# Kernel optimization log

Hardware: AMD Instinct MI355X
Metric: run time of the kernel (lower is better)

## Reference

```python
import jax, jax.numpy as jnp
import numpy as np

N = 8192
IN_DIM = 256
OUT_DIM = 256


def setup_inputs() -> dict:
    key = jax.random.key(0)
    k1, k2, k3, k4 = jax.random.split(key, 4)
    x = jax.random.normal(k1, (N, IN_DIM), dtype=jnp.float32)
    adj = jax.random.uniform(k2, (N, N), dtype=jnp.float32)
    # nn.Linear(in_dim, out_dim): weight [out,in], bias [out]. Store W as [in,out].
    bound = 1.0 / np.sqrt(IN_DIM)
    W = jax.random.uniform(k3, (IN_DIM, OUT_DIM), dtype=jnp.float32, minval=-bound, maxval=bound)
    b = jax.random.uniform(k4, (OUT_DIM,), dtype=jnp.float32, minval=-bound, maxval=bound)
    return {"x": x, "adj": adj, "W": W, "b": b}


def reference(x, adj, W, b):
    # ReLU( D^{-1/2} (A + I) D^{-1/2} X W + b )
    # A_hat = adj + I; degree = A_hat.sum(axis=1)
    n = adj.shape[0]
    A_hat = adj + jnp.eye(n, dtype=adj.dtype)
    degree = A_hat.sum(axis=1)
    d_inv_sqrt = degree ** -0.5  # [N]
    # D^{-1/2} @ A_hat @ D^{-1/2} == row-scale then col-scale (no NxN diag matmuls)
    A_norm = A_hat * d_inv_sqrt[:, None] * d_inv_sqrt[None, :]
    out = A_norm @ x          # [N, in_dim]
    out = out @ W + b         # [N, out_dim]
    return jax.nn.relu(out)
```

## Files before the change

### kernel.cpp

```cpp
#include <hip/hip_runtime.h>
#include <hip/hip_bf16.h>


typedef __attribute__((ext_vector_type(8))) short short8;
typedef __attribute__((ext_vector_type(4))) float floatx4;

#define GLDS16(g, l) __builtin_amdgcn_global_load_lds(\
    (const __attribute__((address_space(1))) void*)(g), \
    (__attribute__((address_space(3))) void*)(l), 16, 0, 0)

__device__ __forceinline__ unsigned short f2b(float f) {
  unsigned int x = __builtin_bit_cast(unsigned int, f);
  unsigned int r = (x + 0x7fffu + ((x >> 16) & 1u)) >> 16;
  return (unsigned short)r;
}

__global__ __launch_bounds__(256) void k_prep(
    const float* __restrict__ adj, float* __restrict__ degree,
    unsigned short* __restrict__ adjb) {
  __shared__ float red[256];
  const int t = threadIdx.x;
  const int bg = blockIdx.x >> 2, kq = blockIdx.x & 3;
  const int m0 = bg * 32;
  const int row = m0 + (t & 31);
  const int kc = t >> 5;
  const float* src = adj + (size_t)row * 8192 + kq * 2048 + kc * 8;
  unsigned short* dst = adjb +
      ((((size_t)(row >> 6)) * 128 + kq * 32) * 512 + kc * 64 + (row & 63)) * 8;
  float rs = 0.f;
#pragma unroll 4
  for (int kt = 0; kt < 32; ++kt) {
    float4 a = *(const float4*)(src + kt * 64);
    float4 b = *(const float4*)(src + kt * 64 + 4);
    rs += a.x + a.y + a.z + a.w + b.x + b.y + b.z + b.w;
    short8 u;
    u[0] = (short)f2b(a.x); u[1] = (short)f2b(a.y);
    u[2] = (short)f2b(a.z); u[3] = (short)f2b(a.w);
    u[4] = (short)f2b(b.x); u[5] = (short)f2b(b.y);
    u[6] = (short)f2b(b.z); u[7] = (short)f2b(b.w);
    *(short8*)(dst + (size_t)kt * 512 * 8) = u;
  }
  red[t] = rs;
  __syncthreads();
  if (t < 32) {
    float sum = red[t] + red[t + 32] + red[t + 64] + red[t + 96] +
                red[t + 128] + red[t + 160] + red[t + 192] + red[t + 224];
    atomicAdd(degree + m0 + t, sum);
  }
}

__global__ __launch_bounds__(256) void k_xw(
    const float* __restrict__ X, const float* __restrict__ W,
    const float* __restrict__ bias, const float* __restrict__ degree,
    float* __restrict__ Zd, unsigned short* __restrict__ Zsb) {
  __shared__ unsigned short ldsT[256 * 36];
  const int t = threadIdx.x, l = t & 63, w = t >> 6;
  const int m0 = blockIdx.x * 32;
  const int r0 = w * 8;
  const int n0 = l * 4;
  const float* Xp = X + (size_t)(m0 + r0) * 256;
  float acc[8][4] = {};
#pragma unroll 2
  for (int k = 0; k < 256; k += 4) {
    float4 wv[4];
#pragma unroll
    for (int j = 0; j < 4; ++j) wv[j] = *(const float4*)(W + (size_t)(k + j) * 256 + n0);
#pragma unroll
    for (int r = 0; r < 8; ++r) {
      float4 xv = *(const float4*)(Xp + r * 256 + k);
      const float xs[4] = {xv.x, xv.y, xv.z, xv.w};
#pragma unroll
      for (int j = 0; j < 4; ++j) {
        acc[r][0] += xs[j] * wv[j].x;
        acc[r][1] += xs[j] * wv[j].y;
        acc[r][2] += xs[j] * wv[j].z;
        acc[r][3] += xs[j] * wv[j].w;
      }
    }
  }
  const float4 bv = *(const float4*)(bias + n0);
  const int kt = m0 >> 6, hh = (m0 >> 5) & 1;
#pragma unroll
  for (int r = 0; r < 8; ++r) {
    const int row = m0 + r0 + r;
    const float sr = rsqrtf(degree[row] + 1.0f);
    float4 zd;
    zd.x = sr * sr * acc[r][0] + bv.x;
    zd.y = sr * sr * acc[r][1] + bv.y;
    zd.z = sr * sr * acc[r][2] + bv.z;
    zd.w = sr * sr * acc[r][3] + bv.w;
    *(float4*)(Zd + (size_t)row * 256 + n0) = zd;
#pragma unroll
    for (int n = 0; n < 4; ++n)
      ldsT[(size_t)(n0 + n) * 36 + (r0 + r)] = f2b(sr * acc[r][n]);
  }
  __syncthreads();
#pragma unroll
  for (int c = 0; c < 4; ++c) {
    const unsigned short* p = ldsT + (size_t)t * 36 + c * 8;
    short8 vv;
#pragma unroll
    for (int j = 0; j < 8; ++j) vv[j] = p[j];
    *(short8*)(Zsb + ((size_t)kt * 2048 + (hh * 4 + c) * 256 + t) * 8) = vv;
  }
}

__global__ __launch_bounds__(512) void k_main(
    const unsigned short* __restrict__ adjb, const unsigned short* __restrict__ Zsb,
    float* __restrict__ P0, float* __restrict__ P1) {
  __shared__ __align__(16) char lds[2][24576];
  const int t = threadIdx.x, l = t & 63, w = t >> 6;
  const int quad = l >> 4, nl = l & 15;
  const int bm = blockIdx.x >> 2, sk = (blockIdx.x >> 1) & 1, nh = blockIdx.x & 1;
  const int wm = w & 1, wn = w >> 1;
  const unsigned short* aBase = adjb + ((size_t)bm * 128 + sk * 64) * 512 * 8;
  const int sl0 = t, sl1 = 512 + t;
  const size_t bU0 = (size_t)(sl0 >> 7) * 256 + nh * 128 + (sl0 & 127);
  const size_t bU1 = (size_t)(sl1 >> 7) * 256 + nh * 128 + (sl1 & 127);
  floatx4 acc[2][2] = {};

  GLDS16(aBase + (size_t)t * 8, lds[0] + t * 16);
  GLDS16(Zsb + ((size_t)(sk * 64) * 2048 + bU0) * 8, lds[0] + 8192 + sl0 * 16);
  GLDS16(Zsb + ((size_t)(sk * 64) * 2048 + bU1) * 8, lds[0] + 8192 + sl1 * 16);
  __syncthreads();

  for (int kt = 0; kt < 64; ++kt) {
    const int cur = kt & 1, nxt = cur ^ 1;
    const int ktn = kt < 63 ? kt + 1 : 63;
    GLDS16(aBase + ((size_t)ktn * 512 + t) * 8, lds[nxt] + t * 16);
    GLDS16(Zsb + ((size_t)(sk * 64 + ktn) * 2048 + bU0) * 8, lds[nxt] + 8192 + sl0 * 16);
    GLDS16(Zsb + ((size_t)(sk * 64 + ktn) * 2048 + bU1) * 8, lds[nxt] + 8192 + sl1 * 16);
    const char* rA = lds[cur];
    const char* rB = lds[cur] + 8192;
#pragma unroll
    for (int kk = 0; kk < 2; ++kk) {
      const int kc = kk * 4 + quad;
      short8 af[2], bf[2];
      af[0] = *(const short8*)(rA + (kc * 64 + wm * 32 + nl) * 16);
      af[1] = *(const short8*)(rA + (kc * 64 + wm * 32 + 16 + nl) * 16);
      bf[0] = *(const short8*)(rB + (kc * 128 + wn * 32 + nl) * 16);
      bf[1] = *(const short8*)(rB + (kc * 128 + wn * 32 + 16 + nl) * 16);
      acc[0][0] = __builtin_amdgcn_mfma_f32_16x16x32_bf16(af[0], bf[0], acc[0][0], 0, 0, 0);
      acc[0][1] = __builtin_amdgcn_mfma_f32_16x16x32_bf16(af[0], bf[1], acc[0][1], 0, 0, 0);
      acc[1][0] = __builtin_amdgcn_mfma_f32_16x16x32_bf16(af[1], bf[0], acc[1][0], 0, 0, 0);
      acc[1][1] = __builtin_amdgcn_mfma_f32_16x16x32_bf16(af[1], bf[1], acc[1][1], 0, 0, 0);
    }
    __syncthreads();
  }

  float* P = sk ? P1 : P0;
#pragma unroll
  for (int mi = 0; mi < 2; ++mi)
#pragma unroll
    for (int ni = 0; ni < 2; ++ni)
#pragma unroll
      for (int r = 0; r < 4; ++r) {
        const int row = bm * 64 + wm * 32 + mi * 16 + quad * 4 + r;
        const int col = nh * 128 + wn * 32 + ni * 16 + nl;
        P[(size_t)row * 256 + col] = acc[mi][ni][r];
      }
}

__global__ __launch_bounds__(256) void k_fin(
    const float* __restrict__ P0, const float* __restrict__ P1,
    const float* __restrict__ Zd, const float* __restrict__ degree,
    float* __restrict__ out) {
  const int i = blockIdx.x * 256 + threadIdx.x;
  const int row = i >> 6;
  const float sr = rsqrtf(degree[row] + 1.0f);
  const float4 p0 = *(const float4*)(P0 + (size_t)i * 4);
  const float4 p1 = *(const float4*)(P1 + (size_t)i * 4);
  const float4 zd = *(const float4*)(Zd + (size_t)i * 4);
  float4 v;
  v.x = sr * (p0.x + p1.x) + zd.x;
  v.y = sr * (p0.y + p1.y) + zd.y;
  v.z = sr * (p0.z + p1.z) + zd.z;
  v.w = sr * (p0.w + p1.w) + zd.w;
  v.x = v.x > 0.f ? v.x : 0.f;
  v.y = v.y > 0.f ? v.y : 0.f;
  v.z = v.z > 0.f ? v.z : 0.f;
  v.w = v.w > 0.f ? v.w : 0.f;
  *(float4*)(out + (size_t)i * 4) = v;
}

extern "C" void kernel_launch(void* const* d_in, const int* in_sizes, int n_in,
                              void* d_out, int out_size, void* d_ws, size_t ws_size,
                              hipStream_t stream) {
  const float* X    = (const float*)d_in[0];
  const float* adj  = (const float*)d_in[1];
  const float* W    = (const float*)d_in[2];
  const float* bias = (const float*)d_in[3];
  float* out = (float*)d_out;
  char* ws = (char*)d_ws;

  float* degree        = (float*)(ws);
  float* Zd            = (float*)(ws + (1 << 20));
  unsigned short* Zsb  = (unsigned short*)(ws + (9 << 20));
  float* P0            = (float*)(ws + (13 << 20));
  float* P1            = (float*)(ws + (21 << 20));
  unsigned short* adjb = (unsigned short*)(ws + ((size_t)29 << 20));

  hipMemsetAsync(degree, 0, 8192 * sizeof(float), stream);
  hipLaunchKernelGGL(k_prep, dim3(1024), dim3(256), 0, stream, adj, degree, adjb);
  hipLaunchKernelGGL(k_xw, dim3(256), dim3(256), 0, stream, X, W, bias, degree, Zd, Zsb);
  hipLaunchKernelGGL(k_main, dim3(512), dim3(512), 0, stream, adjb, Zsb, P0, P1);
  hipLaunchKernelGGL(k_fin, dim3(2048), dim3(256), 0, stream, P0, P1, Zd, degree, out);
}
```

Baseline: 526.5 us.

## Fuse fp32-to-bf16 adjacency conversion into GEMM loads, drop bf16 adj copy

The prep kernel that converted the 256MB fp32 adjacency into a tiled bf16 copy is replaced by a degree-only row-sum kernel using warp shuffles, with no atomics or memset. The main GEMM now reads fp32 adj directly, converts it to bf16 in registers and writes it to a padded LDS layout, with a register prefetch two steps ahead. The work split changes from 2 K-splits by 2 N-halves to 4 K-splits covering all 256 columns, so each adj tile is read once. The aim is to remove the extra write and read of the bf16 adj copy. The cost is that adj is now read twice (degree pass and GEMM), and there are four partial buffers to reduce in the final kernel.

Measured after the change: 509.1 us. -3.3%, faster.

```diff
diff --git a/kernel.cpp b/kernel.cpp
--- a/kernel.cpp
+++ b/kernel.cpp
@@ -15,38 +15,21 @@
   return (unsigned short)r;
 }
 
-__global__ __launch_bounds__(256) void k_prep(
-    const float* __restrict__ adj, float* __restrict__ degree,
-    unsigned short* __restrict__ adjb) {
-  __shared__ float red[256];
+__global__ __launch_bounds__(256) void k_deg(
+    const float* __restrict__ adj, float* __restrict__ degree) {
   const int t = threadIdx.x;
-  const int bg = blockIdx.x >> 2, kq = blockIdx.x & 3;
-  const int m0 = bg * 32;
-  const int row = m0 + (t & 31);
-  const int kc = t >> 5;
-  const float* src = adj + (size_t)row * 8192 + kq * 2048 + kc * 8;
-  unsigned short* dst = adjb +
-      ((((size_t)(row >> 6)) * 128 + kq * 32) * 512 + kc * 64 + (row & 63)) * 8;
+  const int row = blockIdx.x * 8 + (t >> 5);
+  const int c = t & 31;
+  const float* src = adj + (size_t)row * 8192 + c * 4;
   float rs = 0.f;
-#pragma unroll 4
-  for (int kt = 0; kt < 32; ++kt) {
-    float4 a = *(const float4*)(src + kt * 64);
-    float4 b = *(const float4*)(src + kt * 64 + 4);
-    rs += a.x + a.y + a.z + a.w + b.x + b.y + b.z + b.w;
-    short8 u;
-    u[0] = (short)f2b(a.x); u[1] = (short)f2b(a.y);
-    u[2] = (short)f2b(a.z); u[3] = (short)f2b(a.w);
-    u[4] = (short)f2b(b.x); u[5] = (short)f2b(b.y);
-    u[6] = (short)f2b(b.z); u[7] = (short)f2b(b.w);
-    *(short8*)(dst + (size_t)kt * 512 * 8) = u;
-  }
-  red[t] = rs;
-  __syncthreads();
-  if (t < 32) {
-    float sum = red[t] + red[t + 32] + red[t + 64] + red[t + 96] +
-                red[t + 128] + red[t + 160] + red[t + 192] + red[t + 224];
-    atomicAdd(degree + m0 + t, sum);
-  }
+#pragma unroll 8
+  for (int it = 0; it < 64; ++it) {
+    float4 v = *(const float4*)(src + it * 128);
+    rs += v.x + v.y + v.z + v.w;
+  }
+#pragma unroll
+  for (int o = 16; o > 0; o >>= 1) rs += __shfl_down(rs, o, 32);
+  if (c == 0) degree[row] = rs;
 }
 
 __global__ __launch_bounds__(256) void k_xw(
@@ -97,85 +80,110 @@
   __syncthreads();
 #pragma unroll
   for (int c = 0; c < 4; ++c) {
+    const int kcv = hh * 4 + c;
     const unsigned short* p = ldsT + (size_t)t * 36 + c * 8;
     short8 vv;
 #pragma unroll
     for (int j = 0; j < 8; ++j) vv[j] = p[j];
-    *(short8*)(Zsb + ((size_t)kt * 2048 + (hh * 4 + c) * 256 + t) * 8) = vv;
+    *(short8*)(Zsb + ((size_t)kt * 2048 + kcv * 256 + t) * 8) = vv;
   }
 }
 
 __global__ __launch_bounds__(512) void k_main(
-    const unsigned short* __restrict__ adjb, const unsigned short* __restrict__ Zsb,
-    float* __restrict__ P0, float* __restrict__ P1) {
-  __shared__ __align__(16) char lds[2][24576];
+    const float* __restrict__ adj, const unsigned short* __restrict__ Zsb,
+    float* __restrict__ P) {
+  __shared__ __align__(16) char lds[2][20608];
   const int t = threadIdx.x, l = t & 63, w = t >> 6;
   const int quad = l >> 4, nl = l & 15;
-  const int bm = blockIdx.x >> 2, sk = (blockIdx.x >> 1) & 1, nh = blockIdx.x & 1;
+  const int bm = blockIdx.x >> 2, sk = blockIdx.x & 3;
+  const int m0 = bm * 64;
   const int wm = w & 1, wn = w >> 1;
-  const unsigned short* aBase = adjb + ((size_t)bm * 128 + sk * 64) * 512 * 8;
-  const int sl0 = t, sl1 = 512 + t;
-  const size_t bU0 = (size_t)(sl0 >> 7) * 256 + nh * 128 + (sl0 & 127);
-  const size_t bU1 = (size_t)(sl1 >> 7) * 256 + nh * 128 + (sl1 & 127);
-  floatx4 acc[2][2] = {};
-
-  GLDS16(aBase + (size_t)t * 8, lds[0] + t * 16);
-  GLDS16(Zsb + ((size_t)(sk * 64) * 2048 + bU0) * 8, lds[0] + 8192 + sl0 * 16);
-  GLDS16(Zsb + ((size_t)(sk * 64) * 2048 + bU1) * 8, lds[0] + 8192 + sl1 * 16);
+  const int aRow = t >> 3, aCol = t & 7;
+  const float* aSrc = adj + (size_t)(m0 + aRow) * 8192 + sk * 2048 + aCol * 4;
+  const int aOff = (aCol >> 1) * 1040 + aRow * 16 + (aCol & 1) * 8;
+  const unsigned short* bBase = Zsb + (size_t)sk * 65536 * 8;
+  floatx4 acc[2][4] = {};
+
+  float4 avP = *(const float4*)(aSrc);
+#pragma unroll
+  for (int q = 0; q < 2; ++q) {
+    const int sl = q * 512 + t;
+    GLDS16(bBase + (size_t)sl * 8, lds[0] + 4224 + sl * 16);
+  }
+  {
+    unsigned short u0 = f2b(avP.x), u1 = f2b(avP.y), u2 = f2b(avP.z), u3 = f2b(avP.w);
+    unsigned long long pk = (unsigned long long)u0 | ((unsigned long long)u1 << 16)
+                          | ((unsigned long long)u2 << 32) | ((unsigned long long)u3 << 48);
+    *(unsigned long long*)(lds[0] + aOff) = pk;
+  }
+  avP = *(const float4*)(aSrc + 32);
   __syncthreads();
 
-  for (int kt = 0; kt < 64; ++kt) {
-    const int cur = kt & 1, nxt = cur ^ 1;
-    const int ktn = kt < 63 ? kt + 1 : 63;
-    GLDS16(aBase + ((size_t)ktn * 512 + t) * 8, lds[nxt] + t * 16);
-    GLDS16(Zsb + ((size_t)(sk * 64 + ktn) * 2048 + bU0) * 8, lds[nxt] + 8192 + sl0 * 16);
-    GLDS16(Zsb + ((size_t)(sk * 64 + ktn) * 2048 + bU1) * 8, lds[nxt] + 8192 + sl1 * 16);
+  for (int i = 0; i < 64; ++i) {
+    const int cur = i & 1, nxt = cur ^ 1;
+    const int ib = i < 63 ? i + 1 : 63;
+    const int ia = i < 62 ? i + 2 : 63;
+#pragma unroll
+    for (int q = 0; q < 2; ++q) {
+      const int sl = q * 512 + t;
+      GLDS16(bBase + (size_t)(ib * 1024 + sl) * 8, lds[nxt] + 4224 + sl * 16);
+    }
+    float4 avN = *(const float4*)(aSrc + ia * 32);
     const char* rA = lds[cur];
-    const char* rB = lds[cur] + 8192;
-#pragma unroll
-    for (int kk = 0; kk < 2; ++kk) {
-      const int kc = kk * 4 + quad;
-      short8 af[2], bf[2];
-      af[0] = *(const short8*)(rA + (kc * 64 + wm * 32 + nl) * 16);
-      af[1] = *(const short8*)(rA + (kc * 64 + wm * 32 + 16 + nl) * 16);
-      bf[0] = *(const short8*)(rB + (kc * 128 + wn * 32 + nl) * 16);
-      bf[1] = *(const short8*)(rB + (kc * 128 + wn * 32 + 16 + nl) * 16);
-      acc[0][0] = __builtin_amdgcn_mfma_f32_16x16x32_bf16(af[0], bf[0], acc[0][0], 0, 0, 0);
-      acc[0][1] = __builtin_amdgcn_mfma_f32_16x16x32_bf16(af[0], bf[1], acc[0][1], 0, 0, 0);
-      acc[1][0] = __builtin_amdgcn_mfma_f32_16x16x32_bf16(af[1], bf[0], acc[1][0], 0, 0, 0);
-      acc[1][1] = __builtin_amdgcn_mfma_f32_16x16x32_bf16(af[1], bf[1], acc[1][1], 0, 0, 0);
-    }
+    const char* rB = lds[cur] + 4224;
+    short8 af[2], bf[4];
+    af[0] = *(const short8*)(rA + quad * 1040 + (wm * 32 + nl) * 16);
+    af[1] = *(const short8*)(rA + quad * 1040 + (wm * 32 + 16 + nl) * 16);
+#pragma unroll
+    for (int nf = 0; nf < 4; ++nf) {
+      const int col = wn * 64 + nf * 16 + nl;
+      bf[nf] = *(const short8*)(rB + ((size_t)quad * 256 + col) * 16);
+    }
+#pragma unroll
+    for (int mi = 0; mi < 2; ++mi)
+#pragma unroll
+      for (int nf = 0; nf < 4; ++nf)
+        acc[mi][nf] = __builtin_amdgcn_mfma_f32_16x16x32_bf16(af[mi], bf[nf], acc[mi][nf], 0, 0, 0);
+    {
+      unsigned short u0 = f2b(avP.x), u1 = f2b(avP.y), u2 = f2b(avP.z), u3 = f2b(avP.w);
+      unsigned long long pk = (unsigned long long)u0 | ((unsigned long long)u1 << 16)
+                            | ((unsigned long long)u2 << 32) | ((unsigned long long)u3 << 48);
+      *(unsigned long long*)(lds[nxt] + aOff) = pk;
+    }
+    avP = avN;
     __syncthreads();
   }
 
-  float* P = sk ? P1 : P0;
+  float* Pk = P + (size_t)sk * 8192 * 256;
 #pragma unroll
   for (int mi = 0; mi < 2; ++mi)
 #pragma unroll
-    for (int ni = 0; ni < 2; ++ni)
+    for (int nf = 0; nf < 4; ++nf)
 #pragma unroll
       for (int r = 0; r < 4; ++r) {
-        const int row = bm * 64 + wm * 32 + mi * 16 + quad * 4 + r;
-        const int col = nh * 128 + wn * 32 + ni * 16 + nl;
-        P[(size_t)row * 256 + col] = acc[mi][ni][r];
+        const int row = m0 + wm * 32 + mi * 16 + quad * 4 + r;
+        const int col = wn * 64 + nf * 16 + nl;
+        Pk[(size_t)row * 256 + col] = acc[mi][nf][r];
       }
 }
 
 __global__ __launch_bounds__(256) void k_fin(
-    const float* __restrict__ P0, const float* __restrict__ P1,
-    const float* __restrict__ Zd, const float* __restrict__ degree,
-    float* __restrict__ out) {
+    const float* __restrict__ P, const float* __restrict__ Zd,
+    const float* __restrict__ degree, float* __restrict__ out) {
   const int i = blockIdx.x * 256 + threadIdx.x;
   const int row = i >> 6;
   const float sr = rsqrtf(degree[row] + 1.0f);
-  const float4 p0 = *(const float4*)(P0 + (size_t)i * 4);
-  const float4 p1 = *(const float4*)(P1 + (size_t)i * 4);
+  const size_t stride = (size_t)8192 * 256;
+  float4 p0 = *(const float4*)(P + (size_t)i * 4);
+  float4 p1 = *(const float4*)(P + stride + (size_t)i * 4);
+  float4 p2 = *(const float4*)(P + 2 * stride + (size_t)i * 4);
+  float4 p3 = *(const float4*)(P + 3 * stride + (size_t)i * 4);
   const float4 zd = *(const float4*)(Zd + (size_t)i * 4);
   float4 v;
-  v.x = sr * (p0.x + p1.x) + zd.x;
-  v.y = sr * (p0.y + p1.y) + zd.y;
-  v.z = sr * (p0.z + p1.z) + zd.z;
-  v.w = sr * (p0.w + p1.w) + zd.w;
+  v.x = sr * ((p0.x + p1.x) + (p2.x + p3.x)) + zd.x;
+  v.y = sr * ((p0.y + p1.y) + (p2.y + p3.y)) + zd.y;
+  v.z = sr * ((p0.z + p1.z) + (p2.z + p3.z)) + zd.z;
+  v.w = sr * ((p0.w + p1.w) + (p2.w + p3.w)) + zd.w;
   v.x = v.x > 0.f ? v.x : 0.f;
   v.y = v.y > 0.f ? v.y : 0.f;
   v.z = v.z > 0.f ? v.z : 0.f;
@@ -193,16 +201,13 @@
   float* out = (float*)d_out;
   char* ws = (char*)d_ws;
 
-  float* degree        = (float*)(ws);
-  float* Zd            = (float*)(ws + (1 << 20));
-  unsigned short* Zsb  = (unsigned short*)(ws + (9 << 20));
-  float* P0            = (float*)(ws + (13 << 20));
-  float* P1            = (float*)(ws + (21 << 20));
-  unsigned short* adjb = (unsigned short*)(ws + ((size_t)29 << 20));
-
-  hipMemsetAsync(degree, 0, 8192 * sizeof(float), stream);
-  hipLaunchKernelGGL(k_prep, dim3(1024), dim3(256), 0, stream, adj, degree, adjb);
+  float* degree       = (float*)(ws);
+  float* Zd           = (float*)(ws + (1 << 20));
+  unsigned short* Zsb = (unsigned short*)(ws + (9 << 20));
+  float* P            = (float*)(ws + (13 << 20));
+
+  hipLaunchKernelGGL(k_deg, dim3(1024), dim3(256), 0, stream, adj, degree);
   hipLaunchKernelGGL(k_xw, dim3(256), dim3(256), 0, stream, X, W, bias, degree, Zd, Zsb);
-  hipLaunchKernelGGL(k_main, dim3(512), dim3(512), 0, stream, adjb, Zsb, P0, P1);
-  hipLaunchKernelGGL(k_fin, dim3(2048), dim3(256), 0, stream, P0, P1, Zd, degree, out);
-}
+  hipLaunchKernelGGL(k_main, dim3(512), dim3(512), 0, stream, adj, Zsb, P);
+  hipLaunchKernelGGL(k_fin, dim3(2048), dim3(256), 0, stream, P, Zd, degree, out);
+}
```
